# Kernel optimization log

Measured on AMD Instinct MI355X. Metric: run time of the kernel, lower is better.

The kernel has to match this reference:

```python
import jax, jax.numpy as jnp
import numpy as np

N_MEL = 80
NEG = -1e30  # log-zero sentinel, as in the torch module


def setup_inputs() -> dict:
    key = jax.random.key(0)
    k1, k2, k3, k4 = jax.random.split(key, 4)
    B, txt_T, mel_T = 16, 128, 512
    mu_logvar = jax.random.normal(k1, (B, txt_T, 2 * N_MEL), dtype=jnp.float32)
    melspec = jax.random.normal(k2, (B, N_MEL, mel_T), dtype=jnp.float32)
    text_lengths = jax.random.randint(k3, (B,), txt_T // 2, txt_T + 1, dtype=jnp.int32)
    mel_lengths = jax.random.randint(k4, (B,), mel_T // 2, mel_T + 1, dtype=jnp.int32)
    return dict(mu_logvar=mu_logvar, melspec=melspec,
                text_lengths=text_lengths, mel_lengths=mel_lengths)


def _log_prob_matrix(mu_logvar, melspec):
    # mu_logvar: [B, txt_T, 2*n_mel]; melspec: [B, n_mel, mel_T]
    mu = mu_logvar[:, :, :N_MEL]            # [B, txt_T, n_mel]
    logvar = mu_logvar[:, :, N_MEL:]        # [B, txt_T, n_mel]
    x = jnp.transpose(melspec, (0, 2, 1))   # [B, mel_T, n_mel]
    diff = x[:, None, :, :] - mu[:, :, None, :]          # [B, txt_T, mel_T, n_mel]
    quad = diff * diff * jnp.exp(-logvar)[:, :, None, :] + logvar[:, :, None, :]
    return -0.5 * jnp.mean(quad, axis=3)    # [B, txt_T, mel_T]


def _log_alpha_last(log_prob_matrix, text_lengths, mel_lengths):
    B, txt_T, mel_T = log_prob_matrix.shape
    # init: log_alpha[:, :, 0] = NEG except [:,0,0] = logp[:,0,0]
    init = jnp.full((B, txt_T), NEG, log_prob_matrix.dtype).at[:, 0].set(log_prob_matrix[:, 0, 0])
    logp_t = jnp.moveaxis(log_prob_matrix, 2, 0)  # [mel_T, B, txt_T]

    def step(prev, lp):
        # shift-by-one along text axis (monotonic alignment: stay or advance)
        shifted = jnp.concatenate([jnp.full((B, 1), NEG, prev.dtype), prev[:, :-1]], axis=1)
        cur = jnp.logaddexp(prev + 1e-30, shifted + 1e-30) + lp
        return cur, cur

    _, rest = jax.lax.scan(step, init, logp_t[1:])
    log_alpha = jnp.concatenate([init[None], rest], axis=0)  # [mel_T, B, txt_T]
    b = jnp.arange(B)
    return log_alpha[mel_lengths - 1, b, text_lengths - 1]   # [B]


def reference(mu_logvar, melspec, text_lengths, mel_lengths):
    log_prob_matrix = _log_prob_matrix(mu_logvar, melspec)
    alpha_last = _log_alpha_last(log_prob_matrix, text_lengths, mel_lengths)
    alpha_last = alpha_last / mel_lengths
    mdn_loss = -jnp.mean(alpha_last)
    return (mdn_loss, log_prob_matrix)
```

## Files before the change

kernel.cpp:

```cpp
#include <hip/hip_runtime.h>

#define NEG  (-1e30f)
#define LN2F 0.69314718056f

#define B_   16
#define TXT_ 128
#define MEL_ 512
#define NM_  80
#define IT_  8

typedef float vf2 __attribute__((ext_vector_type(2)));

__global__ __launch_bounds__(512) void lp_kernel(
    const float* __restrict__ mu_logvar,
    const float* __restrict__ melspec,
    float* __restrict__ lp_out,
    float* __restrict__ wT,
    float* __restrict__ out0)
{
    const int i0 = blockIdx.x * IT_;
    const int b  = blockIdx.y;
    const int t  = threadIdx.x;

    __shared__ float2 s_wb[IT_][NM_];
    __shared__ float  s_cp[IT_ * NM_];
    __shared__ float  s_cc[IT_];

    for (int u = t; u < IT_ * NM_; u += 512) {
        int ii = u / NM_;
        int n  = u - ii * NM_;
        const float* row = mu_logvar + (size_t)(b * TXT_ + i0 + ii) * (2 * NM_);
        float mu = row[n];
        float lv = row[NM_ + n];
        float w  = __expf(-lv);
        s_wb[ii][n] = make_float2(w, -2.f * mu * w);
        s_cp[u]     = mu * mu * w + lv;
    }
    __syncthreads();
    if (t < IT_) {
        float c = 0.f;
        #pragma unroll
        for (int n = 0; n < NM_; ++n) c += s_cp[t * NM_ + n];
        s_cc[t] = c;
    }
    __syncthreads();

    const float* xcol = melspec + (size_t)b * NM_ * MEL_ + t;
    float acc[IT_];
    #pragma unroll
    for (int ii = 0; ii < IT_; ++ii) acc[ii] = 0.f;

    #pragma unroll 4
    for (int n = 0; n < NM_; ++n) {
        float x  = xcol[(size_t)n * MEL_];
        float x2 = x * x;
        #pragma unroll
        for (int ii = 0; ii < IT_; ++ii) {
            float2 wb = s_wb[ii][n];
            acc[ii] = fmaf(wb.x, x2, fmaf(wb.y, x, acc[ii]));
        }
    }

    const size_t rowbase = ((size_t)(b * TXT_ + i0)) * MEL_ + t;
    #pragma unroll
    for (int ii = 0; ii < IT_; ++ii) {
        lp_out[rowbase + (size_t)ii * MEL_] =
            (-0.5f / (float)NM_) * (acc[ii] + s_cc[ii]);
    }

    if (i0 == 0 && t == 0) wT[(size_t)b * MEL_ * TXT_] = 0.f;
    if (i0 == 0 && b == 0 && t == 0) *out0 = 0.f;
}

__global__ __launch_bounds__(256) void wt_kernel(
    const float* __restrict__ lp,
    const int* __restrict__ mel_len,
    float* __restrict__ wT)
{
    __shared__ float tileT[32][TXT_ + 1];
    __shared__ float pmax[32][8];
    __shared__ float psum[32];

    const int t0  = blockIdx.x * 32;
    const int b   = blockIdx.y;
    const int tid = threadIdx.x;

    const float* src = lp + (size_t)b * TXT_ * MEL_ + t0;
    for (int u = tid; u < TXT_ * 32; u += 256) {
        int i = u >> 5, c = u & 31;
        tileT[c][i] = src[(size_t)i * MEL_ + c];
    }
    __syncthreads();

    {
        int tt = tid >> 3, g = tid & 7;
        float m = NEG;
        #pragma unroll
        for (int k = 0; k < 16; ++k) m = fmaxf(m, tileT[tt][g * 16 + k]);
        pmax[tt][g] = m;
    }
    __syncthreads();
    if (tid < 32) {
        float m = pmax[tid][0];
        #pragma unroll
        for (int g = 1; g < 8; ++g) m = fmaxf(m, pmax[tid][g]);
        pmax[tid][0] = m;
        int tg = t0 + tid;
        int TendM1 = mel_len[b] - 1;
        psum[tid] = (tg >= 1 && tg <= TendM1) ? (m + LN2F) : 0.f;
    }
    __syncthreads();

    float* dstb = wT + (size_t)b * MEL_ * TXT_;
    for (int u = tid; u < 32 * TXT_; u += 256) {
        int tt = u >> 7, i = u & 127;
        int tg = t0 + tt;
        if (tg != 0)
            dstb[(size_t)tg * TXT_ + i] =
                __expf(tileT[tt][i] - pmax[tt][0] - LN2F);
    }

    if (tid == 0) {
        float s = 0.f;
        #pragma unroll
        for (int k = 0; k < 32; ++k) s += psum[k];
        if (t0 == 0) s += tileT[0][0];
        atomicAdd(&dstb[0], s);
    }
}

__device__ __forceinline__ float dpp_shr1_zero(float x) {
    int r = __builtin_amdgcn_update_dpp(
        0, __builtin_bit_cast(int, x), 0x138 , 0xf, 0xf, false);
    return __builtin_bit_cast(float, r);
}

#define DPPMAX(M, CTRL, RM)                                               \
    do {                                                                  \
        int _t = __builtin_amdgcn_update_dpp(                             \
            __builtin_bit_cast(int, M), __builtin_bit_cast(int, M),       \
            CTRL, RM, 0xf, false);                                        \
        M = fmaxf(M, __builtin_bit_cast(float, _t));                      \
    } while (0)

#define GLOAD2(DST, PTR) \
    asm volatile("global_load_dwordx2 %0, %1, off" : "=v"(DST) : "v"(PTR))
#define VWAIT44(A,B,C,D2) \
    asm volatile("s_waitcnt vmcnt(44)" : "+v"(A), "+v"(B), "+v"(C), "+v"(D2))

__global__ __launch_bounds__(64) void scan_kernel(
    const float* __restrict__ wT,
    const int* __restrict__ text_len, const int* __restrict__ mel_len,
    float* __restrict__ out0)
{
    const int b = blockIdx.x;
    const int l = threadIdx.x;
    const float* base = wT + (size_t)b * MEL_ * TXT_;
    const float* wb_  = base + 2 * l;
    const int Tend = mel_len[b], TendM1 = Tend - 1;

    float s0 = (l == 0) ? 1.f : 0.f;
    float s1 = 0.f;
    float fin0 = 0.f, fin1 = 0.f;
    int   shift_acc = 0, fsh = 0;
    int   t_cur = 1;
    int   t_pf  = 49;

    vf2 q0,q1,q2,q3,q4,q5,q6,q7,q8,q9,q10,q11,q12,q13,q14,q15,
        q16,q17,q18,q19,q20,q21,q22,q23,q24,q25,q26,q27,q28,q29,q30,q31,
        q32,q33,q34,q35,q36,q37,q38,q39,q40,q41,q42,q43,q44,q45,q46,q47;
    {
        const float* p;
        #define INIT(Q, ROW) p = wb_ + (size_t)(ROW) * TXT_; GLOAD2(Q, p)
        INIT(q0,1);   INIT(q1,2);   INIT(q2,3);   INIT(q3,4);
        INIT(q4,5);   INIT(q5,6);   INIT(q6,7);   INIT(q7,8);
        INIT(q8,9);   INIT(q9,10);  INIT(q10,11); INIT(q11,12);
        INIT(q12,13); INIT(q13,14); INIT(q14,15); INIT(q15,16);
        INIT(q16,17); INIT(q17,18); INIT(q18,19); INIT(q19,20);
        INIT(q20,21); INIT(q21,22); INIT(q22,23); INIT(q23,24);
        INIT(q24,25); INIT(q25,26); INIT(q26,27); INIT(q27,28);
        INIT(q28,29); INIT(q29,30); INIT(q30,31); INIT(q31,32);
        INIT(q32,33); INIT(q33,34); INIT(q34,35); INIT(q35,36);
        INIT(q36,37); INIT(q37,38); INIT(q38,39); INIT(q39,40);
        INIT(q40,41); INIT(q41,42); INIT(q42,43); INIT(q43,44);
        INIT(q44,45); INIT(q45,46); INIT(q46,47); INIT(q47,48);
        #undef INIT
    }

    #define STEP(Q)                                          \
        do {                                                 \
            float nb  = dpp_shr1_zero(s1);                   \
            float ns0 = (s0 + nb) * (Q).x;                   \
            float ns1 = (s1 + s0) * (Q).y;                   \
            bool hit = (t_cur == TendM1);                    \
            fin0 = hit ? ns0 : fin0;                         \
            fin1 = hit ? ns1 : fin1;                         \
            fsh  = hit ? shift_acc : fsh;                    \
            s0 = ns0; s1 = ns1; ++t_cur;                     \
        } while (0)

    #define REFILL(Q)                                        \
        do {                                                 \
            int rr = min(t_pf, MEL_ - 1);                    \
            const float* p_ = wb_ + (size_t)rr * TXT_;       \
            GLOAD2(Q, p_);                                   \
            ++t_pf;                                          \
        } while (0)

    #define GROUP(QA,QB,QC,QD)                               \
        do {                                                 \
            VWAIT44(QA,QB,QC,QD);                            \
            STEP(QA); STEP(QB); STEP(QC); STEP(QD);          \
            REFILL(QA); REFILL(QB); REFILL(QC); REFILL(QD);  \
        } while (0)

    #define RENORM16()                                                    \
        do {                                                              \
            float mm = fmaxf(s0, s1);                                     \
            DPPMAX(mm, 0x111, 0xf);                       \
            DPPMAX(mm, 0x112, 0xf);                       \
            DPPMAX(mm, 0x114, 0xf);                       \
            DPPMAX(mm, 0x118, 0xf);                       \
            DPPMAX(mm, 0x142, 0xa);         \
            DPPMAX(mm, 0x143, 0xc);         \
            float M = __builtin_bit_cast(                                 \
                float, __builtin_amdgcn_readlane(                         \
                           __builtin_bit_cast(int, mm), 63));             \
            if (M > 0.f) {                                                \
                int e;                                                    \
                (void)frexpf(M, &e);                                      \
                float sc = ldexpf(1.f, -e);                               \
                s0 *= sc; s1 *= sc;                                       \
                shift_acc += e;                                           \
            }                                                             \
        } while (0)

    for (int t0 = 1; t0 <= TendM1; t0 += 48) {
        GROUP(q0,q1,q2,q3);     GROUP(q4,q5,q6,q7);
        GROUP(q8,q9,q10,q11);   GROUP(q12,q13,q14,q15);
        RENORM16();
        GROUP(q16,q17,q18,q19); GROUP(q20,q21,q22,q23);
        GROUP(q24,q25,q26,q27); GROUP(q28,q29,q30,q31);
        RENORM16();
        GROUP(q32,q33,q34,q35); GROUP(q36,q37,q38,q39);
        GROUP(q40,q41,q42,q43); GROUP(q44,q45,q46,q47);
        RENORM16();
    }
    #undef STEP
    #undef REFILL
    #undef GROUP
    #undef RENORM16

    int jstar = text_len[b] - 1;
    float vs = (jstar & 1) ? fin1 : fin0;
    int   vh = fsh;
    vs = __shfl(vs, jstar >> 1);
    vh = __shfl(vh, jstar >> 1);
    if (l == 0) {
        float musum = base[0];
        float val   = __logf(vs) + (float)vh * LN2F + musum;
        atomicAdd(out0, -(val / (float)Tend) * (1.f / (float)B_));
    }
}

extern "C" void kernel_launch(void* const* d_in, const int* in_sizes, int n_in,
                              void* d_out, int out_size, void* d_ws, size_t ws_size,
                              hipStream_t stream) {
    const float* mu_logvar = (const float*)d_in[0];
    const float* melspec   = (const float*)d_in[1];
    const int*   text_len  = (const int*)d_in[2];
    const int*   mel_len   = (const int*)d_in[3];

    float* out    = (float*)d_out;
    float* lp_out = out + 1;
    float* wT     = (float*)d_ws;

    dim3 g1(TXT_ / IT_, B_);
    lp_kernel<<<g1, MEL_, 0, stream>>>(mu_logvar, melspec, lp_out, wT, out);
    dim3 g2(MEL_ / 32, B_);
    wt_kernel<<<g2, 256, 0, stream>>>(lp_out, mel_len, wT);
    scan_kernel<<<B_, 64, 0, stream>>>(wT, text_len, mel_len, out);
}
```

Baseline: 103.9 us.

## Fuse weight transform into scan kernel with fp16 LDS ring buffer

Removes the separate wt_kernel and its global workspace round trip. The scan kernel now runs 512 threads per batch: each thread loads one mel column, computes its max, and writes exp weights as packed half2 into a swizzled three-chunk LDS ring. Wave 0 runs the recurrence out of LDS while the other waves fill later chunks. This saves a launch and global traffic, but it stores the weights in fp16, which lowers precision, and it needs a block-wide sync per chunk plus 128 registers per thread for the column values.

```diff
diff --git a/kernel.cpp b/kernel.cpp
--- a/kernel.cpp
+++ b/kernel.cpp
@@ -1,4 +1,5 @@
 #include <hip/hip_runtime.h>
+#include <hip/hip_fp16.h>
 
 #define NEG  (-1e30f)
 #define LN2F 0.69314718056f
@@ -9,13 +10,16 @@
 #define NM_  80
 #define IT_  8
 
+#define CH_   80
+#define NCH_  7
+#define CHD_  (CH_ * 64)
+
 typedef float vf2 __attribute__((ext_vector_type(2)));
 
 __global__ __launch_bounds__(512) void lp_kernel(
     const float* __restrict__ mu_logvar,
     const float* __restrict__ melspec,
     float* __restrict__ lp_out,
-    float* __restrict__ wT,
     float* __restrict__ out0)
 {
     const int i0 = blockIdx.x * IT_;
@@ -68,65 +72,7 @@
             (-0.5f / (float)NM_) * (acc[ii] + s_cc[ii]);
     }
 
-    if (i0 == 0 && t == 0) wT[(size_t)b * MEL_ * TXT_] = 0.f;
     if (i0 == 0 && b == 0 && t == 0) *out0 = 0.f;
-}
-
-__global__ __launch_bounds__(256) void wt_kernel(
-    const float* __restrict__ lp,
-    const int* __restrict__ mel_len,
-    float* __restrict__ wT)
-{
-    __shared__ float tileT[32][TXT_ + 1];
-    __shared__ float pmax[32][8];
-    __shared__ float psum[32];
-
-    const int t0  = blockIdx.x * 32;
-    const int b   = blockIdx.y;
-    const int tid = threadIdx.x;
-
-    const float* src = lp + (size_t)b * TXT_ * MEL_ + t0;
-    for (int u = tid; u < TXT_ * 32; u += 256) {
-        int i = u >> 5, c = u & 31;
-        tileT[c][i] = src[(size_t)i * MEL_ + c];
-    }
-    __syncthreads();
-
-    {
-        int tt = tid >> 3, g = tid & 7;
-        float m = NEG;
-        #pragma unroll
-        for (int k = 0; k < 16; ++k) m = fmaxf(m, tileT[tt][g * 16 + k]);
-        pmax[tt][g] = m;
-    }
-    __syncthreads();
-    if (tid < 32) {
-        float m = pmax[tid][0];
-        #pragma unroll
-        for (int g = 1; g < 8; ++g) m = fmaxf(m, pmax[tid][g]);
-        pmax[tid][0] = m;
-        int tg = t0 + tid;
-        int TendM1 = mel_len[b] - 1;
-        psum[tid] = (tg >= 1 && tg <= TendM1) ? (m + LN2F) : 0.f;
-    }
-    __syncthreads();
-
-    float* dstb = wT + (size_t)b * MEL_ * TXT_;
-    for (int u = tid; u < 32 * TXT_; u += 256) {
-        int tt = u >> 7, i = u & 127;
-        int tg = t0 + tt;
-        if (tg != 0)
-            dstb[(size_t)tg * TXT_ + i] =
-                __expf(tileT[tt][i] - pmax[tt][0] - LN2F);
-    }
-
-    if (tid == 0) {
-        float s = 0.f;
-        #pragma unroll
-        for (int k = 0; k < 32; ++k) s += psum[k];
-        if (t0 == 0) s += tileT[0][0];
-        atomicAdd(&dstb[0], s);
-    }
 }
 
 __device__ __forceinline__ float dpp_shr1_zero(float x) {
@@ -143,76 +89,85 @@
         M = fmaxf(M, __builtin_bit_cast(float, _t));                      \
     } while (0)
 
-#define GLOAD2(DST, PTR) \
-    asm volatile("global_load_dwordx2 %0, %1, off" : "=v"(DST) : "v"(PTR))
-#define VWAIT44(A,B,C,D2) \
-    asm volatile("s_waitcnt vmcnt(44)" : "+v"(A), "+v"(B), "+v"(C), "+v"(D2))
-
-__global__ __launch_bounds__(64) void scan_kernel(
-    const float* __restrict__ wT,
+__global__ __launch_bounds__(512) void fused_scan(
+    const float* __restrict__ lp,
     const int* __restrict__ text_len, const int* __restrict__ mel_len,
     float* __restrict__ out0)
 {
+    __shared__ unsigned int wbuf[3 * CHD_];
+    __shared__ float wsum[8];
+    __shared__ float s_lp00;
+
     const int b = blockIdx.x;
-    const int l = threadIdx.x;
-    const float* base = wT + (size_t)b * MEL_ * TXT_;
-    const float* wb_  = base + 2 * l;
+    const int t = threadIdx.x;
+    const int l = t;
+    const float* col = lp + (size_t)b * TXT_ * MEL_ + t;
+
     const int Tend = mel_len[b], TendM1 = Tend - 1;
+
+    float vv[TXT_];
+    float m = NEG;
+    #pragma unroll
+    for (int p = 0; p < TXT_; ++p) {
+        float f = col[(size_t)p * MEL_];
+        vv[p] = f;
+        m = fmaxf(m, f);
+    }
+    const float mu_t = m + LN2F;
+
+    float contrib = (t >= 1 && t <= TendM1) ? mu_t : 0.f;
+    #pragma unroll
+    for (int off = 32; off; off >>= 1) contrib += __shfl_down(contrib, off);
+    if ((t & 63) == 0) wsum[t >> 6] = contrib;
+    if (t == 0) s_lp00 = vv[0];
+
+    const int myc  = t / CH_;
+    const int rloc = t - myc * CH_;
+    unsigned int* wb = wbuf + (myc % 3) * CHD_ + rloc * 64;
+    const int swz = t & 31;
+
+    #define WRITEW()                                                      \
+        do {                                                              \
+            _Pragma("unroll")                                             \
+            for (int p = 0; p < 64; ++p) {                                \
+                float e0 = __expf(vv[2 * p]     - mu_t);                  \
+                float e1 = __expf(vv[2 * p + 1] - mu_t);                  \
+                wb[p ^ swz] = __builtin_bit_cast(                         \
+                    unsigned int, __floats2half2_rn(e0, e1));             \
+            }                                                             \
+        } while (0)
+
+    if (myc <= 1) WRITEW();
+    __syncthreads();
 
     float s0 = (l == 0) ? 1.f : 0.f;
     float s1 = 0.f;
     float fin0 = 0.f, fin1 = 0.f;
     int   shift_acc = 0, fsh = 0;
-    int   t_cur = 1;
-    int   t_pf  = 49;
-
-    vf2 q0,q1,q2,q3,q4,q5,q6,q7,q8,q9,q10,q11,q12,q13,q14,q15,
-        q16,q17,q18,q19,q20,q21,q22,q23,q24,q25,q26,q27,q28,q29,q30,q31,
-        q32,q33,q34,q35,q36,q37,q38,q39,q40,q41,q42,q43,q44,q45,q46,q47;
-    {
-        const float* p;
-        #define INIT(Q, ROW) p = wb_ + (size_t)(ROW) * TXT_; GLOAD2(Q, p)
-        INIT(q0,1);   INIT(q1,2);   INIT(q2,3);   INIT(q3,4);
-        INIT(q4,5);   INIT(q5,6);   INIT(q6,7);   INIT(q7,8);
-        INIT(q8,9);   INIT(q9,10);  INIT(q10,11); INIT(q11,12);
-        INIT(q12,13); INIT(q13,14); INIT(q14,15); INIT(q15,16);
-        INIT(q16,17); INIT(q17,18); INIT(q18,19); INIT(q19,20);
-        INIT(q20,21); INIT(q21,22); INIT(q22,23); INIT(q23,24);
-        INIT(q24,25); INIT(q25,26); INIT(q26,27); INIT(q27,28);
-        INIT(q28,29); INIT(q29,30); INIT(q30,31); INIT(q31,32);
-        INIT(q32,33); INIT(q33,34); INIT(q34,35); INIT(q35,36);
-        INIT(q36,37); INIT(q37,38); INIT(q38,39); INIT(q39,40);
-        INIT(q40,41); INIT(q41,42); INIT(q42,43); INIT(q43,44);
-        INIT(q44,45); INIT(q45,46); INIT(q46,47); INIT(q47,48);
-        #undef INIT
-    }
-
-    #define STEP(Q)                                          \
-        do {                                                 \
-            float nb  = dpp_shr1_zero(s1);                   \
-            float ns0 = (s0 + nb) * (Q).x;                   \
-            float ns1 = (s1 + s0) * (Q).y;                   \
-            bool hit = (t_cur == TendM1);                    \
-            fin0 = hit ? ns0 : fin0;                         \
-            fin1 = hit ? ns1 : fin1;                         \
-            fsh  = hit ? shift_acc : fsh;                    \
-            s0 = ns0; s1 = ns1; ++t_cur;                     \
-        } while (0)
-
-    #define REFILL(Q)                                        \
-        do {                                                 \
-            int rr = min(t_pf, MEL_ - 1);                    \
-            const float* p_ = wb_ + (size_t)rr * TXT_;       \
-            GLOAD2(Q, p_);                                   \
-            ++t_pf;                                          \
-        } while (0)
-
-    #define GROUP(QA,QB,QC,QD)                               \
-        do {                                                 \
-            VWAIT44(QA,QB,QC,QD);                            \
-            STEP(QA); STEP(QB); STEP(QC); STEP(QD);          \
-            REFILL(QA); REFILL(QB); REFILL(QC); REFILL(QD);  \
-        } while (0)
+    vf2 A[16], Bq[16];
+
+    #define LOADN(ARR, RL0, N)                                            \
+        _Pragma("unroll")                                                 \
+        for (int j = 0; j < (N); ++j) {                                   \
+            int rl = (RL0) + j;                                           \
+            unsigned int u_ = bb[rl * 64 + (l ^ ((lo + rl) & 31))];       \
+            float2 f_ = __half22float2(__builtin_bit_cast(__half2, u_));  \
+            ARR[j].x = f_.x; ARR[j].y = f_.y;                             \
+        }
+
+    #define STEPN(ARR, RL0, N)                                            \
+        _Pragma("unroll")                                                 \
+        for (int j = 0; j < (N); ++j) {                                   \
+            int row = lo + (RL0) + j;                                     \
+            float nb  = dpp_shr1_zero(s1);                                \
+            float ns0 = (s0 + nb) * ARR[j].x;                             \
+            float ns1 = (s1 + s0) * ARR[j].y;                             \
+            bool hit = (row == TendM1);                                   \
+            fin0 = hit ? ns0 : fin0;                                      \
+            fin1 = hit ? ns1 : fin1;                                      \
+            fsh  = hit ? shift_acc : fsh;                                 \
+            s0 = ns0; s1 = ns1;                                           \
+        }
 
     #define RENORM16()                                                    \
         do {                                                              \
@@ -235,31 +190,52 @@
             }                                                             \
         } while (0)
 
-    for (int t0 = 1; t0 <= TendM1; t0 += 48) {
-        GROUP(q0,q1,q2,q3);     GROUP(q4,q5,q6,q7);
-        GROUP(q8,q9,q10,q11);   GROUP(q12,q13,q14,q15);
-        RENORM16();
-        GROUP(q16,q17,q18,q19); GROUP(q20,q21,q22,q23);
-        GROUP(q24,q25,q26,q27); GROUP(q28,q29,q30,q31);
-        RENORM16();
-        GROUP(q32,q33,q34,q35); GROUP(q36,q37,q38,q39);
-        GROUP(q40,q41,q42,q43); GROUP(q44,q45,q46,q47);
-        RENORM16();
-    }
-    #undef STEP
-    #undef REFILL
-    #undef GROUP
+    for (int c = 0; c < NCH_; ++c) {
+        if (t < 64) {
+            const unsigned int* bb = wbuf + (c % 3) * CHD_;
+            const int lo = c * CH_;
+            if (c == 0) {
+                LOADN(A, 1, 15); LOADN(Bq, 16, 16);
+                STEPN(A, 1, 15);  RENORM16();
+                LOADN(A, 32, 16); STEPN(Bq, 16, 16); RENORM16();
+                LOADN(Bq, 48, 16); STEPN(A, 32, 16); RENORM16();
+                LOADN(A, 64, 16); STEPN(Bq, 48, 16); RENORM16();
+                STEPN(A, 64, 16); RENORM16();
+            } else if (c < 6) {
+                LOADN(A, 0, 16); LOADN(Bq, 16, 16);
+                STEPN(A, 0, 16);  RENORM16();
+                LOADN(A, 32, 16); STEPN(Bq, 16, 16); RENORM16();
+                LOADN(Bq, 48, 16); STEPN(A, 32, 16); RENORM16();
+                LOADN(A, 64, 16); STEPN(Bq, 48, 16); RENORM16();
+                STEPN(A, 64, 16); RENORM16();
+            } else {
+                LOADN(A, 0, 16); LOADN(Bq, 16, 16);
+                STEPN(A, 0, 16);  RENORM16();
+                STEPN(Bq, 16, 16); RENORM16();
+            }
+        } else if (myc == c + 2) {
+            WRITEW();
+        }
+        __syncthreads();
+    }
+    #undef LOADN
+    #undef STEPN
     #undef RENORM16
-
-    int jstar = text_len[b] - 1;
-    float vs = (jstar & 1) ? fin1 : fin0;
-    int   vh = fsh;
-    vs = __shfl(vs, jstar >> 1);
-    vh = __shfl(vh, jstar >> 1);
-    if (l == 0) {
-        float musum = base[0];
-        float val   = __logf(vs) + (float)vh * LN2F + musum;
-        atomicAdd(out0, -(val / (float)Tend) * (1.f / (float)B_));
+    #undef WRITEW
+
+    if (t < 64) {
+        int jstar = text_len[b] - 1;
+        float vs = (jstar & 1) ? fin1 : fin0;
+        int   vh = fsh;
+        vs = __shfl(vs, jstar >> 1);
+        vh = __shfl(vh, jstar >> 1);
+        if (l == 0) {
+            float ms = 0.f;
+            #pragma unroll
+            for (int k = 0; k < 8; ++k) ms += wsum[k];
+            float val = __logf(vs) + (float)vh * LN2F + ms + s_lp00;
+            atomicAdd(out0, -(val / (float)Tend) * (1.f / (float)B_));
+        }
     }
 }
 
@@ -273,11 +249,9 @@
 
     float* out    = (float*)d_out;
     float* lp_out = out + 1;
-    float* wT     = (float*)d_ws;
+    (void)d_ws; (void)ws_size;
 
     dim3 g1(TXT_ / IT_, B_);
-    lp_kernel<<<g1, MEL_, 0, stream>>>(mu_logvar, melspec, lp_out, wT, out);
-    dim3 g2(MEL_ / 32, B_);
-    wt_kernel<<<g2, 256, 0, stream>>>(lp_out, mel_len, wT);
-    scan_kernel<<<B_, 64, 0, stream>>>(wT, text_len, mel_len, out);
-}
+    lp_kernel<<<g1, MEL_, 0, stream>>>(mu_logvar, melspec, lp_out, out);
+    fused_scan<<<B_, 512, 0, stream>>>(lp_out, text_len, mel_len, out);
+}
```

New measurement: 171.6 us. +65.2%, slower.

## Store scan weights as packed fp16 pairs and restructure scan prefetch pipeline

Applied to the files above, without the earlier changes.

The wt kernel now writes the exponentiated transition weights as half2-packed values. Two time steps are interleaved into each 8-byte load per lane, so the sequential scan fetches half the bytes per step and keeps 24 loads in flight instead of 48. The per-batch mean-shift sum moves to a separate small buffer, and renormalisation now uses exponent bit manipulation in place of frexp/ldexp and runs more often. This trades fp16 precision on the weights, which are normalised to at most about 0.5 per column, for less memory latency in the latency-bound scan.

```diff
diff --git a/kernel.cpp b/kernel.cpp
--- a/kernel.cpp
+++ b/kernel.cpp
@@ -1,4 +1,5 @@
 #include <hip/hip_runtime.h>
+#include <hip/hip_fp16.h>
 
 #define NEG  (-1e30f)
 #define LN2F 0.69314718056f
@@ -11,11 +12,12 @@
 
 typedef float vf2 __attribute__((ext_vector_type(2)));
 
+
 __global__ __launch_bounds__(512) void lp_kernel(
     const float* __restrict__ mu_logvar,
     const float* __restrict__ melspec,
     float* __restrict__ lp_out,
-    float* __restrict__ wT,
+    float* __restrict__ musum,
     float* __restrict__ out0)
 {
     const int i0 = blockIdx.x * IT_;
@@ -68,64 +70,74 @@
             (-0.5f / (float)NM_) * (acc[ii] + s_cc[ii]);
     }
 
-    if (i0 == 0 && t == 0) wT[(size_t)b * MEL_ * TXT_] = 0.f;
+    if (i0 == 0 && t == 0) musum[b] = 0.f;
     if (i0 == 0 && b == 0 && t == 0) *out0 = 0.f;
 }
 
 __global__ __launch_bounds__(256) void wt_kernel(
     const float* __restrict__ lp,
     const int* __restrict__ mel_len,
-    float* __restrict__ wT)
+    float* __restrict__ musum,
+    uint2* __restrict__ wp)
 {
     __shared__ float tileT[32][TXT_ + 1];
     __shared__ float pmax[32][8];
     __shared__ float psum[32];
 
-    const int t0  = blockIdx.x * 32;
+    const int x   = blockIdx.x;
+    const int t0  = x * 32;
     const int b   = blockIdx.y;
     const int tid = threadIdx.x;
 
-    const float* src = lp + (size_t)b * TXT_ * MEL_ + t0;
+    const float* src = lp + (size_t)b * TXT_ * MEL_;
     for (int u = tid; u < TXT_ * 32; u += 256) {
         int i = u >> 5, c = u & 31;
-        tileT[c][i] = src[(size_t)i * MEL_ + c];
+        int tg = min(t0 + 1 + c, MEL_ - 1);
+        tileT[c][i] = src[(size_t)i * MEL_ + tg];
     }
     __syncthreads();
 
     {
-        int tt = tid >> 3, g = tid & 7;
+        int cc = tid >> 3, g = tid & 7;
         float m = NEG;
         #pragma unroll
-        for (int k = 0; k < 16; ++k) m = fmaxf(m, tileT[tt][g * 16 + k]);
-        pmax[tt][g] = m;
+        for (int k = 0; k < 16; ++k) m = fmaxf(m, tileT[cc][g * 16 + k]);
+        pmax[cc][g] = m;
     }
     __syncthreads();
     if (tid < 32) {
         float m = pmax[tid][0];
         #pragma unroll
         for (int g = 1; g < 8; ++g) m = fmaxf(m, pmax[tid][g]);
-        pmax[tid][0] = m;
-        int tg = t0 + tid;
+        float mu = m + LN2F;
+        pmax[tid][0] = mu;
+        int tg = t0 + 1 + tid;
         int TendM1 = mel_len[b] - 1;
-        psum[tid] = (tg >= 1 && tg <= TendM1) ? (m + LN2F) : 0.f;
-    }
-    __syncthreads();
-
-    float* dstb = wT + (size_t)b * MEL_ * TXT_;
-    for (int u = tid; u < 32 * TXT_; u += 256) {
-        int tt = u >> 7, i = u & 127;
-        int tg = t0 + tt;
-        if (tg != 0)
-            dstb[(size_t)tg * TXT_ + i] =
-                __expf(tileT[tt][i] - pmax[tt][0] - LN2F);
+        psum[tid] = (tg <= TendM1) ? mu : 0.f;
+    }
+    __syncthreads();
+
+    uint2* dst = wp + ((size_t)b * 256 + (t0 >> 1)) * 64;
+    for (int u = tid; u < 16 * 64; u += 256) {
+        int ul = u >> 6, l = u & 63;
+        float m0 = pmax[2 * ul][0];
+        float m1 = pmax[2 * ul + 1][0];
+        float a0 = __expf(tileT[2 * ul][2 * l]     - m0);
+        float a1 = __expf(tileT[2 * ul][2 * l + 1] - m0);
+        float b0 = __expf(tileT[2 * ul + 1][2 * l]     - m1);
+        float b1 = __expf(tileT[2 * ul + 1][2 * l + 1] - m1);
+        uint2 q;
+        q.x = __builtin_bit_cast(unsigned int, __floats2half2_rn(a0, a1));
+        q.y = __builtin_bit_cast(unsigned int, __floats2half2_rn(b0, b1));
+        dst[(size_t)ul * 64 + l] = q;
     }
 
     if (tid == 0) {
         float s = 0.f;
         #pragma unroll
         for (int k = 0; k < 32; ++k) s += psum[k];
-        if (t0 == 0) s += tileT[0][0];
-        atomicAdd(&dstb[0], s);
+        if (x == 0) s += src[0];
+        atomicAdd(&musum[b], s);
     }
 }
 
@@ -145,18 +157,18 @@
 
 #define GLOAD2(DST, PTR) \
     asm volatile("global_load_dwordx2 %0, %1, off" : "=v"(DST) : "v"(PTR))
-#define VWAIT44(A,B,C,D2) \
-    asm volatile("s_waitcnt vmcnt(44)" : "+v"(A), "+v"(B), "+v"(C), "+v"(D2))
+#define VWAIT20(A,B,C,D2) \
+    asm volatile("s_waitcnt vmcnt(20)" : "+v"(A), "+v"(B), "+v"(C), "+v"(D2))
 
 __global__ __launch_bounds__(64) void scan_kernel(
-    const float* __restrict__ wT,
+    const uint2* __restrict__ wp,
+    const float* __restrict__ musum,
     const int* __restrict__ text_len, const int* __restrict__ mel_len,
     float* __restrict__ out0)
 {
     const int b = blockIdx.x;
     const int l = threadIdx.x;
-    const float* base = wT + (size_t)b * MEL_ * TXT_;
-    const float* wb_  = base + 2 * l;
+    const uint2* pb = wp + (size_t)b * 256 * 64 + l;
     const int Tend = mel_len[b], TendM1 = Tend - 1;
 
     float s0 = (l == 0) ? 1.f : 0.f;
@@ -164,34 +176,27 @@
     float fin0 = 0.f, fin1 = 0.f;
     int   shift_acc = 0, fsh = 0;
     int   t_cur = 1;
-    int   t_pf  = 49;
-
-    vf2 q0,q1,q2,q3,q4,q5,q6,q7,q8,q9,q10,q11,q12,q13,q14,q15,
-        q16,q17,q18,q19,q20,q21,q22,q23,q24,q25,q26,q27,q28,q29,q30,q31,
-        q32,q33,q34,q35,q36,q37,q38,q39,q40,q41,q42,q43,q44,q45,q46,q47;
+    int   u_pf  = 24;
+
+    vf2 q0,q1,q2,q3,q4,q5,q6,q7,q8,q9,q10,q11,
+        q12,q13,q14,q15,q16,q17,q18,q19,q20,q21,q22,q23;
     {
-        const float* p;
-        #define INIT(Q, ROW) p = wb_ + (size_t)(ROW) * TXT_; GLOAD2(Q, p)
-        INIT(q0,1);   INIT(q1,2);   INIT(q2,3);   INIT(q3,4);
-        INIT(q4,5);   INIT(q5,6);   INIT(q6,7);   INIT(q7,8);
-        INIT(q8,9);   INIT(q9,10);  INIT(q10,11); INIT(q11,12);
-        INIT(q12,13); INIT(q13,14); INIT(q14,15); INIT(q15,16);
-        INIT(q16,17); INIT(q17,18); INIT(q18,19); INIT(q19,20);
-        INIT(q20,21); INIT(q21,22); INIT(q22,23); INIT(q23,24);
-        INIT(q24,25); INIT(q25,26); INIT(q26,27); INIT(q27,28);
-        INIT(q28,29); INIT(q29,30); INIT(q30,31); INIT(q31,32);
-        INIT(q32,33); INIT(q33,34); INIT(q34,35); INIT(q35,36);
-        INIT(q36,37); INIT(q37,38); INIT(q38,39); INIT(q39,40);
-        INIT(q40,41); INIT(q41,42); INIT(q42,43); INIT(q43,44);
-        INIT(q44,45); INIT(q45,46); INIT(q46,47); INIT(q47,48);
+        #define INIT(Q, U) do { const uint2* p_ = pb + (size_t)(U) * 64; \
+                                GLOAD2(Q, p_); } while (0)
+        INIT(q0,0);   INIT(q1,1);   INIT(q2,2);   INIT(q3,3);
+        INIT(q4,4);   INIT(q5,5);   INIT(q6,6);   INIT(q7,7);
+        INIT(q8,8);   INIT(q9,9);   INIT(q10,10); INIT(q11,11);
+        INIT(q12,12); INIT(q13,13); INIT(q14,14); INIT(q15,15);
+        INIT(q16,16); INIT(q17,17); INIT(q18,18); INIT(q19,19);
+        INIT(q20,20); INIT(q21,21); INIT(q22,22); INIT(q23,23);
         #undef INIT
     }
 
-    #define STEP(Q)                                          \
+    #define STEP1(WX, WY)                                    \
         do {                                                 \
             float nb  = dpp_shr1_zero(s1);                   \
-            float ns0 = (s0 + nb) * (Q).x;                   \
-            float ns1 = (s1 + s0) * (Q).y;                   \
+            float ns0 = (s0 + nb) * (WX);                    \
+            float ns1 = (s1 + s0) * (WY);                    \
             bool hit = (t_cur == TendM1);                    \
             fin0 = hit ? ns0 : fin0;                         \
             fin1 = hit ? ns1 : fin1;                         \
@@ -199,18 +204,26 @@
             s0 = ns0; s1 = ns1; ++t_cur;                     \
         } while (0)
 
+    #define STEP2(Q)                                                      \
+        do {                                                              \
+            float2 fa = __half22float2(__builtin_bit_cast(__half2, (Q).x)); \
+            float2 fb = __half22float2(__builtin_bit_cast(__half2, (Q).y)); \
+            STEP1(fa.x, fa.y);                                            \
+            STEP1(fb.x, fb.y);                                            \
+        } while (0)
+
     #define REFILL(Q)                                        \
         do {                                                 \
-            int rr = min(t_pf, MEL_ - 1);                    \
-            const float* p_ = wb_ + (size_t)rr * TXT_;       \
+            int ru = min(u_pf, 255);                         \
+            const uint2* p_ = pb + (size_t)ru * 64;          \
             GLOAD2(Q, p_);                                   \
-            ++t_pf;                                          \
+            ++u_pf;                                          \
         } while (0)
 
     #define GROUP(QA,QB,QC,QD)                               \
         do {                                                 \
-            VWAIT44(QA,QB,QC,QD);                            \
-            STEP(QA); STEP(QB); STEP(QC); STEP(QD);          \
+            VWAIT20(QA,QB,QC,QD);                            \
+            STEP2(QA); STEP2(QB); STEP2(QC); STEP2(QD);      \
             REFILL(QA); REFILL(QB); REFILL(QC); REFILL(QD);  \
         } while (0)
 
@@ -223,30 +236,25 @@
             DPPMAX(mm, 0x118, 0xf);                       \
             DPPMAX(mm, 0x142, 0xa);         \
             DPPMAX(mm, 0x143, 0xc);         \
-            float M = __builtin_bit_cast(                                 \
-                float, __builtin_amdgcn_readlane(                         \
-                           __builtin_bit_cast(int, mm), 63));             \
-            if (M > 0.f) {                                                \
-                int e;                                                    \
-                (void)frexpf(M, &e);                                      \
-                float sc = ldexpf(1.f, -e);                               \
+            int ib = __builtin_amdgcn_readlane(                           \
+                         __builtin_bit_cast(int, mm), 63);                \
+            int be = (ib >> 23) & 0xff;                                   \
+            if (be > 0) {                                                 \
+                float sc = __builtin_bit_cast(float, (253 - be) << 23);   \
                 s0 *= sc; s1 *= sc;                                       \
-                shift_acc += e;                                           \
+                shift_acc += be - 126;                                    \
             }                                                             \
         } while (0)
 
-    for (int t0 = 1; t0 <= TendM1; t0 += 48) {
-        GROUP(q0,q1,q2,q3);     GROUP(q4,q5,q6,q7);
-        GROUP(q8,q9,q10,q11);   GROUP(q12,q13,q14,q15);
-        RENORM16();
-        GROUP(q16,q17,q18,q19); GROUP(q20,q21,q22,q23);
-        GROUP(q24,q25,q26,q27); GROUP(q28,q29,q30,q31);
-        RENORM16();
-        GROUP(q32,q33,q34,q35); GROUP(q36,q37,q38,q39);
-        GROUP(q40,q41,q42,q43); GROUP(q44,q45,q46,q47);
-        RENORM16();
-    }
-    #undef STEP
+    const int G = (TendM1 + 7) >> 3;
+    #pragma unroll 1
+    for (int gg = 0; gg < G; gg += 6) {
+        GROUP(q0,q1,q2,q3);     GROUP(q4,q5,q6,q7);     RENORM16();
+        GROUP(q8,q9,q10,q11);   GROUP(q12,q13,q14,q15); RENORM16();
+        GROUP(q16,q17,q18,q19); GROUP(q20,q21,q22,q23); RENORM16();
+    }
+    #undef STEP1
+    #undef STEP2
     #undef REFILL
     #undef GROUP
     #undef RENORM16
@@ -257,8 +265,7 @@
     vs = __shfl(vs, jstar >> 1);
     vh = __shfl(vh, jstar >> 1);
     if (l == 0) {
-        float musum = base[0];
-        float val   = __logf(vs) + (float)vh * LN2F + musum;
+        float val = __logf(vs) + (float)vh * LN2F + musum[b];
         atomicAdd(out0, -(val / (float)Tend) * (1.f / (float)B_));
     }
 }
@@ -273,11 +280,12 @@
 
     float* out    = (float*)d_out;
     float* lp_out = out + 1;
-    float* wT     = (float*)d_ws;
+    float* musum  = (float*)d_ws;
+    uint2* wp     = (uint2*)((char*)d_ws + 256);
 
     dim3 g1(TXT_ / IT_, B_);
-    lp_kernel<<<g1, MEL_, 0, stream>>>(mu_logvar, melspec, lp_out, wT, out);
+    lp_kernel<<<g1, MEL_, 0, stream>>>(mu_logvar, melspec, lp_out, musum, out);
     dim3 g2(MEL_ / 32, B_);
-    wt_kernel<<<g2, 256, 0, stream>>>(lp_out, mel_len, wT);
-    scan_kernel<<<B_, 64, 0, stream>>>(wT, text_len, mel_len, out);
-}
+    wt_kernel<<<g2, 256, 0, stream>>>(lp_out, mel_len, musum, wp);
+    scan_kernel<<<B_, 64, 0, stream>>>(wp, musum, text_len, mel_len, out);
+}
```

Result: no change. 103.7 us (-0.2%).
